# Kernel tuning notes

Measured on AMD Instinct MI355X. Metric: run time of the kernel, lower is better.

## Reference

```python
import jax, jax.numpy as jnp
import numpy as np

# Config (from init_kwargs 'knn')
QUEUE_SIZE = 65536   # K
FEAT_DIM = 256       # D
BATCH = 512          # N (eval_sampling = 1.0 -> all samples used)
NUM_KNNS = 200
NUM_CLASSES = 1000
TEMPERATURE = 0.07


def _l2norm(x):
    return x / jnp.sqrt(jnp.sum(x * x, axis=-1, keepdims=True) + 1e-12)


def setup_inputs() -> dict:
    key = jax.random.key(0)
    k1, k2, k3, k4 = jax.random.split(key, 4)
    features = _l2norm(jax.random.normal(k1, (BATCH, FEAT_DIM), jnp.float32))
    labels = jax.random.randint(k2, (BATCH,), 0, NUM_CLASSES, jnp.int32)
    queue_features = _l2norm(jax.random.normal(k3, (QUEUE_SIZE, FEAT_DIM), jnp.float32))
    queue_labels = jax.random.randint(k4, (QUEUE_SIZE,), 0, NUM_CLASSES, jnp.int32)
    return {
        "features": features,
        "labels": labels,
        "queue_features": queue_features,
        "queue_labels": queue_labels,
        "queue_ptr": 0,
    }


def reference(features, labels, queue_features, queue_labels, queue_ptr):
    # ---- kNN accuracy (train branch, eval_sampling=1.0) ----
    sim = jnp.einsum('nc,kc->nk', features, queue_features)           # [N, K]
    sim_w, sim_idx = jax.lax.top_k(sim, k=NUM_KNNS)                   # [N, Kn]
    sim_w = jnp.exp(sim_w / TEMPERATURE)
    sim_labels = queue_labels[sim_idx]                                # [N, Kn] (vmapped gather)
    # weighted one-hot vote, expressed as a scatter-add (same math,
    # avoids the [N, Kn, C] one-hot intermediate)
    n = features.shape[0]
    pred_scores = jnp.zeros((n, NUM_CLASSES), sim_w.dtype)
    pred_scores = pred_scores.at[jnp.arange(n)[:, None], sim_labels].add(sim_w)
    pred_labels = jnp.argmax(pred_scores, axis=-1)
    accuracy = jnp.mean((pred_labels == labels).astype(jnp.float32))

    # ---- queue update (single device: all_gather == identity) ----
    batch_size = features.shape[0]
    inds = (jnp.arange(batch_size) + queue_ptr) % QUEUE_SIZE  # original asserts divisibility
    new_queue_features = queue_features.at[inds].set(features)
    new_queue_labels = queue_labels.at[inds].set(labels)
    new_queue_ptr = (queue_ptr + batch_size) % QUEUE_SIZE

    return accuracy, new_queue_features, new_queue_labels, new_queue_ptr
```

## Files before the change

### kernel.cpp

```cpp
#include <hip/hip_runtime.h>
#include <math.h>

#define NQ     65536
#define DIM    256
#define NBATCH 512
#define KNN    200
#define NCLS   1000
#define TSELF  0.155f
#define TSELH  0.150f
#define BGUARD 22

#define GM  128
#define GK  32
#define NTN (NQ / GM)
#define KSTEPS (DIM / GK)

typedef unsigned short u16;
typedef unsigned long long u64;
typedef __attribute__((ext_vector_type(8))) short short8;
typedef __attribute__((ext_vector_type(4))) float f32x4;


__device__ __forceinline__ u16 f2bf(float x) {
  unsigned u = __float_as_uint(x);
  return (u16)((u + 0x7FFFu + ((u >> 16) & 1u)) >> 16);
}
__device__ __forceinline__ void load_lds16(const void* g, void* l) {
  __builtin_amdgcn_global_load_lds(
      (const __attribute__((address_space(1))) unsigned int*)g,
      (__attribute__((address_space(3))) unsigned int*)l, 16, 0, 0);
}
__device__ __forceinline__ void store_f4u(float* p, float4 v) {
  p[0] = v.x;
  *(float2*)(p + 1) = make_float2(v.y, v.z);
  p[3] = v.w;
}

__global__ __launch_bounds__(256) void prep_copy_kernel(
    const float* __restrict__ feat, const int* __restrict__ labels,
    const float* __restrict__ qf, const int* __restrict__ ql,
    const int* __restrict__ qptr,
    u16* __restrict__ Bb, u16* __restrict__ Ab,
    int* __restrict__ flag, float* __restrict__ out)
{
  const int idx = blockIdx.x * 256 + threadIdx.x;
  const int ptr = qptr[0];
  const long long NFEAT = (long long)NQ * DIM;

  {
    float4 qv = ((const float4*)qf)[idx];
    int row = idx >> 6;
    int c4  = idx & 63;
    int d = (row - ptr) & (NQ - 1);
    float4 ov = qv;
    if (d < NBATCH) ov = ((const float4*)feat)[d * 64 + c4];
    store_f4u(out + 1 + 4 * (long long)idx, ov);

    ushort4 h;
    h.x = f2bf(qv.x); h.y = f2bf(qv.y); h.z = f2bf(qv.z); h.w = f2bf(qv.w);
    ((ushort4*)Bb)[idx] = h;
  }

  if (idx < NBATCH * DIM / 4) {
    float4 v = ((const float4*)feat)[idx];
    ushort4 h;
    h.x = f2bf(v.x); h.y = f2bf(v.y); h.z = f2bf(v.z); h.w = f2bf(v.w);
    ((ushort4*)Ab)[idx] = h;
  }

  if (idx < NQ) {
    int d = (idx - ptr) & (NQ - 1);
    int v = (d < NBATCH) ? labels[d] : ql[idx];
    out[1 + NFEAT + idx] = (float)v;
  }

  if (idx < NBATCH) flag[idx] = 0;
  if (idx == 0) {
    out[0] = 0.0f;
    out[1 + NFEAT + NQ] = (float)((ptr + NBATCH) & (NQ - 1));
  }
}

__global__ __launch_bounds__(256) void gemm_mfma(
    const u16* __restrict__ A, const u16* __restrict__ B,
    unsigned* __restrict__ cand, int* __restrict__ cnt2,
    int* __restrict__ flag, int SLOT)
{
  __shared__ u16 sA[2][GM][GK];
  __shared__ u16 sB[2][GM][GK];
  __shared__ int lcnt[GM];

  const int tid  = threadIdx.x;
  const int wave = tid >> 6, lane = tid & 63;
  const int d  = blockIdx.x;
  const int bm = (d >> 3) & 3;
  const int bn = (d & 7) | ((d >> 5) << 3);

  for (int i = tid; i < GM; i += 256) lcnt[i] = 0;

  const u16* srcBase = ((wave < 2) ? (A + (size_t)bm * GM * DIM)
                                   : (B + (size_t)bn * GM * DIM))
                       + (size_t)(wave & 1) * 64 * DIM;
  const int kx = ((lane & 3) ^ ((lane >> 3) & 3)) * 8;
  const u16* src = srcBase + (lane >> 2) * DIM + kx;
  u16* dst0 = ((wave < 2) ? &sA[0][0][0] : &sB[0][0][0]) + (wave & 1) * 64 * GK;
  u16* dst1 = ((wave < 2) ? &sA[1][0][0] : &sB[1][0][0]) + (wave & 1) * 64 * GK;

  const int wm = (wave & 1) * 64, wn = (wave >> 1) * 64;
  const int fr = lane & 15;
  const int fq = lane >> 4;
  const int fqx = fq ^ ((fr >> 1) & 3);

  f32x4 acc[4][4] = {};

  {
    const u16* s = src;
#pragma unroll
    for (int g = 0; g < 4; ++g)
      load_lds16(s + g * 16 * DIM, dst0 + g * 512);
  }
  __syncthreads();

  for (int t = 0; t < KSTEPS; ++t) {
    const int cur = t & 1;
    if (t + 1 < KSTEPS) {
      const u16* s = src + (t + 1) * GK;
      u16* dl = cur ? dst0 : dst1;
#pragma unroll
      for (int g = 0; g < 4; ++g)
        load_lds16(s + g * 16 * DIM, dl + g * 512);
    }

    short8 a[4], b[4];
#pragma unroll
    for (int i = 0; i < 4; ++i) {
      a[i] = *(const short8*)&sA[cur][wm + i * 16 + fr][fqx * 8];
      b[i] = *(const short8*)&sB[cur][wn + i * 16 + fr][fqx * 8];
    }
#pragma unroll
    for (int i = 0; i < 4; ++i)
#pragma unroll
      for (int j = 0; j < 4; ++j)
        acc[i][j] = __builtin_amdgcn_mfma_f32_16x16x32_bf16(a[i], b[j], acc[i][j], 0, 0, 0);

    __syncthreads();
  }

  const int lrow0 = wm + fq * 4;
  const int ccol  = bn * GM + wn + fr;
#pragma unroll
  for (int i = 0; i < 4; ++i)
#pragma unroll
    for (int j = 0; j < 4; ++j)
#pragma unroll
      for (int r = 0; r < 4; ++r) {
        float v = acc[i][j][r];
        if (v > TSELF) {
          int lr  = lrow0 + i * 16 + r;
          int col = ccol + j * 16;
          int p = atomicAdd(&lcnt[lr], 1);
          if (p < SLOT)
            cand[((size_t)(bm * GM + lr) * NTN + bn) * SLOT + p] = (unsigned)col;
          else
            flag[bm * GM + lr] = 1;
        }
      }
  __syncthreads();
  if (tid < GM) {
    int c = lcnt[tid];
    cnt2[(size_t)(bm * GM + tid) * NTN + bn] = c < SLOT ? c : SLOT;
  }
}

#define NBSEL 2048
#define CCAP  2048
#define MBCAP 256
#define NT    512
#define NG    (NT / 8)

__global__ __launch_bounds__(NT, 4) void select_kernel(
    const unsigned* __restrict__ cand, const int* __restrict__ cnt2,
    const int* __restrict__ flag, const int* __restrict__ labels,
    const int* __restrict__ qlab, const float* __restrict__ qf,
    const float* __restrict__ feat, float* __restrict__ out,
    float inv_n, int SLOT)
{
  __shared__ int   hist[NBSEL];
  __shared__ int   seg[NT];
  __shared__ float candV[CCAP];
  __shared__ int   candI[CCAP];
  __shared__ float votes[NCLS];
  __shared__ u64   bk[MBCAP];
  __shared__ float frow[DIM];
  __shared__ int   s_b, s_cnt, s_hi, s_mb;
  __shared__ u64   s_best;

  const int tid = threadIdx.x;
  const int row = blockIdx.x;

  bool fb = (flag[row] != 0);

  if (tid < DIM) frow[tid] = feat[(size_t)row * DIM + tid];
  for (int i = tid; i < NBSEL; i += NT) hist[i] = 0;
  for (int c = tid; c < NCLS; c += NT) votes[c] = 0.0f;
  if (tid == 0) { s_b = 0; s_cnt = 0; s_hi = 0; s_mb = 0; s_best = 0ull; }
  __syncthreads();

  if (!fb) {
    const int*      rowcnt  = cnt2 + (size_t)row * NTN;
    const unsigned* rowcand = cand + (size_t)row * NTN * SLOT;
    for (int t = tid; t < NTN; t += NT) {
      int c = rowcnt[t];
      if (c > 0) {
        int p = atomicAdd(&s_cnt, c);
        for (int k = 0; k < c; ++k)
          if (p + k < CCAP) candI[p + k] = (int)rowcand[(size_t)t * SLOT + k];
      }
    }
    __syncthreads();
    const int n = s_cnt;
    if (n < KNN || n > CCAP) fb = true;
    else {
      const int sub = tid & 7;
      const int grp = tid >> 3;
      const float4* fr4 = (const float4*)frow;

      float4 b0[8];
      if (grp < n) {
        const float4* qr = (const float4*)(qf + (size_t)candI[grp] * DIM);
#pragma unroll
        for (int it = 0; it < 8; ++it) b0[it] = qr[sub + it * 8];
      }
      for (int i = grp; i < n; i += NG) {
        const int j = i + NG;
        float4 b1[8];
        if (j < n) {
          const float4* qr = (const float4*)(qf + (size_t)candI[j] * DIM);
#pragma unroll
          for (int it = 0; it < 8; ++it) b1[it] = qr[sub + it * 8];
        }
        float p = 0.0f;
#pragma unroll
        for (int it = 0; it < 8; ++it) {
          float4 a = fr4[sub + it * 8];
          p = fmaf(a.x, b0[it].x, p); p = fmaf(a.y, b0[it].y, p);
          p = fmaf(a.z, b0[it].z, p); p = fmaf(a.w, b0[it].w, p);
        }
        p += __shfl_xor(p, 1, 64);
        p += __shfl_xor(p, 2, 64);
        p += __shfl_xor(p, 4, 64);
        if (sub == 0) candV[i] = p;
#pragma unroll
        for (int it = 0; it < 8; ++it) b0[it] = b1[it];
      }
      __syncthreads();

      const float SSCALE = (float)NBSEL / (1.001f - TSELH);
      for (int i = tid; i < n; i += NT) {
        int b = (int)((candV[i] - TSELH) * SSCALE);
        b = b < 0 ? 0 : (b > NBSEL - 1 ? NBSEL - 1 : b);
        atomicAdd(&hist[b], 1);
      }
      __syncthreads();
      { int s = 0;
#pragma unroll
        for (int i = 0; i < NBSEL / NT; ++i) s += hist[tid * (NBSEL / NT) + i];
        seg[tid] = s; }
      __syncthreads();
      for (int off = 1; off < NT; off <<= 1) {
        int t = (tid + off < NT) ? seg[tid + off] : 0;
        __syncthreads();
        seg[tid] += t;
        __syncthreads();
      }
      { int run = (tid < NT - 1) ? seg[tid + 1] : 0;
        for (int i = tid * (NBSEL / NT) + NBSEL / NT - 1;
             i >= tid * (NBSEL / NT); --i) {
          run += hist[i];
          if (run >= KNN) { atomicMax(&s_b, i); break; }
        } }
      __syncthreads();
      const int bstar = s_b;

      if (bstar < BGUARD) fb = true;
      else {
        for (int i = tid; i < n; i += NT) {
          float v = candV[i];
          int b = (int)((v - TSELH) * SSCALE);
          b = b < 0 ? 0 : (b > NBSEL - 1 ? NBSEL - 1 : b);
          if (b > bstar) {
            atomicAdd(&s_hi, 1);
            atomicAdd(&votes[qlab[candI[i]]], expf(v * (1.0f / 0.07f)));
          } else if (b == bstar) {
            int p = atomicAdd(&s_mb, 1);
            if (p < MBCAP)
              bk[p] = ((u64)__float_as_uint(v) << 32) |
                      (u64)(0xFFFFFFFFu - (unsigned)candI[i]);
          }
        }
        __syncthreads();
        const int mb = s_mb;
        if (mb > MBCAP) fb = true;
        else {
          const int need = KNN - s_hi;
          for (int e = tid; e < mb; e += NT) {
            u64 ke = bk[e];
            int rank = 0;
            for (int j = 0; j < mb; ++j) rank += (bk[j] > ke);
            if (rank < need) {
              float v = __uint_as_float((unsigned)(ke >> 32));
              int col = (int)(0xFFFFFFFFu - (unsigned)(ke & 0xFFFFFFFFull));
              atomicAdd(&votes[qlab[col]], expf(v * (1.0f / 0.07f)));
            }
          }
          __syncthreads();
        }
      }
    }
  }

  if (fb) {
    for (int i = tid; i < NBSEL; i += NT) hist[i] = 0;
    if (tid == 0) { s_b = 0; s_cnt = 0; }
    __syncthreads();

    for (int q = tid; q < NQ; q += NT) {
      const float4* qr = (const float4*)(qf + (size_t)q * DIM);
      const float4* fr = (const float4*)frow;
      float s = 0.0f;
#pragma unroll
      for (int t = 0; t < DIM / 4; ++t) {
        float4 a = fr[t], b = qr[t];
        s = fmaf(a.x, b.x, s); s = fmaf(a.y, b.y, s);
        s = fmaf(a.z, b.z, s); s = fmaf(a.w, b.w, s);
      }
      int bin = (int)((s + 1.0f) * (NBSEL * 0.5f));
      bin = bin < 0 ? 0 : (bin > NBSEL - 1 ? NBSEL - 1 : bin);
      atomicAdd(&hist[bin], 1);
    }
    __syncthreads();

    { int s = 0;
#pragma unroll
      for (int i = 0; i < NBSEL / NT; ++i) s += hist[tid * (NBSEL / NT) + i];
      seg[tid] = s; }
    __syncthreads();
    for (int off = 1; off < NT; off <<= 1) {
      int t = (tid + off < NT) ? seg[tid + off] : 0;
      __syncthreads();
      seg[tid] += t;
      __syncthreads();
    }
    { int run = (tid < NT - 1) ? seg[tid + 1] : 0;
      for (int i = tid * (NBSEL / NT) + NBSEL / NT - 1;
           i >= tid * (NBSEL / NT); --i) {
        run += hist[i];
        if (run >= KNN) { atomicMax(&s_b, i); break; }
      } }
    __syncthreads();
    const int bstar = s_b;

    for (int q = tid; q < NQ; q += NT) {
      const float4* qr = (const float4*)(qf + (size_t)q * DIM);
      const float4* fr = (const float4*)frow;
      float s = 0.0f;
#pragma unroll
      for (int t = 0; t < DIM / 4; ++t) {
        float4 a = fr[t], b = qr[t];
        s = fmaf(a.x, b.x, s); s = fmaf(a.y, b.y, s);
        s = fmaf(a.z, b.z, s); s = fmaf(a.w, b.w, s);
      }
      int bin = (int)((s + 1.0f) * (NBSEL * 0.5f));
      bin = bin < 0 ? 0 : (bin > NBSEL - 1 ? NBSEL - 1 : bin);
      if (bin >= bstar) {
        int p = atomicAdd(&s_cnt, 1);
        if (p < CCAP) { candV[p] = s; candI[p] = q; }
      }
    }
    __syncthreads();
    int m = s_cnt < CCAP ? s_cnt : CCAP;

    int P = 256; while (P < m) P <<= 1;
    for (int i = tid; i < P; i += NT)
      if (i >= m) { candV[i] = -INFINITY; candI[i] = 0x7fffffff; }
    __syncthreads();
    for (int k = 2; k <= P; k <<= 1) {
      for (int j = k >> 1; j > 0; j >>= 1) {
        for (int i = tid; i < P; i += NT) {
          int ixj = i ^ j;
          if (ixj > i) {
            float va = candV[i], vb = candV[ixj];
            int ia = candI[i], ib = candI[ixj];
            bool aFirst = (va > vb) || (va == vb && ia < ib);
            bool up = ((i & k) == 0);
            if (up ? !aFirst : aFirst) {
              candV[i] = vb; candV[ixj] = va;
              candI[i] = ib; candI[ixj] = ia;
            }
          }
        }
        __syncthreads();
      }
    }

    for (int c = tid; c < NCLS; c += NT) votes[c] = 0.0f;
    __syncthreads();
    for (int i = tid; i < KNN; i += NT)
      atomicAdd(&votes[qlab[candI[i]]], expf(candV[i] * (1.0f / 0.07f)));
    __syncthreads();
  }

  u64 key = 0ull;
  for (int c = tid; c < NCLS; c += NT) {
    u64 k2 = ((u64)__float_as_uint(votes[c]) << 32) |
             (u64)(0xFFFFFFFFu - (unsigned)c);
    if (k2 > key) key = k2;
  }
  for (int off = 32; off > 0; off >>= 1) {
    u64 o = __shfl_down(key, off, 64);
    if (o > key) key = o;
  }
  if ((tid & 63) == 0) atomicMax(&s_best, key);
  __syncthreads();
  if (tid == 0) {
    int cls = (int)(0xFFFFFFFFu - (unsigned)(s_best & 0xFFFFFFFFull));
    if (cls == labels[row]) atomicAdd(out, inv_n);
  }
}

extern "C" void kernel_launch(void* const* d_in, const int* in_sizes, int n_in,
                              void* d_out, int out_size, void* d_ws, size_t ws_size,
                              hipStream_t stream)
{
  const float* features = (const float*)d_in[0];
  const int*   labels   = (const int*)d_in[1];
  const float* qfeat    = (const float*)d_in[2];
  const int*   qlab     = (const int*)d_in[3];
  const int*   qptr     = (const int*)d_in[4];
  float* out = (float*)d_out;

  int nbatch = in_sizes[0] / DIM;
  float inv_n = 1.0f / (float)nbatch;

  size_t bBytes = (size_t)NQ * DIM * 2;
  size_t fixed  = bBytes + (size_t)NBATCH * NTN * 4 + NBATCH * 4 +
                  (size_t)NBATCH * DIM * 2;
  int SLOT = 16;
  while ((size_t)NBATCH * NTN * SLOT * 4 + fixed > ws_size && SLOT > 2) SLOT >>= 1;

  u16*      Bb   = (u16*)d_ws;
  unsigned* cand = (unsigned*)((char*)d_ws + bBytes);
  int*      cnt2 = (int*)((char*)cand + (size_t)NBATCH * NTN * SLOT * 4);
  int*      flagp = cnt2 + (size_t)NBATCH * NTN;
  u16*      Ab   = (u16*)(flagp + NBATCH);

  prep_copy_kernel<<<NQ * DIM / 4 / 256, 256, 0, stream>>>(
      features, labels, qfeat, qlab, qptr, Bb, Ab, flagp, out);

  gemm_mfma<<<(NBATCH / GM) * (NQ / GM), 256, 0, stream>>>(
      Ab, Bb, cand, cnt2, flagp, SLOT);

  select_kernel<<<nbatch, NT, 0, stream>>>(cand, cnt2, flagp, labels, qlab,
                                           qfeat, features, out, inv_n, SLOT);
}
```

Baseline: 201.3 us.

## Reuse bf16 GEMM scores to pre-rank candidates, rescore only near-threshold ones in fp32

The GEMM now stores each candidate's bf16 similarity next to its column index. The select kernel builds a histogram from these approximate scores to find a provisional cutoff, keeps only candidates within an error margin of it, and recomputes exact fp32 dot products for that short list before the final exact histogram selection. This cuts the number of gathered 1 KB queue rows and dot products per query, but doubles the candidate buffer size and adds a second histogram and scan pass. Correctness relies on the bf16 error bound EPSF being large enough.

Measured after the change: 200.7 us, median of 2. Within noise of the previous version (-0.3%).

```diff
diff --git a/kernel.cpp b/kernel.cpp
--- a/kernel.cpp
+++ b/kernel.cpp
@@ -8,6 +8,7 @@
 #define NCLS   1000
 #define TSELF  0.155f
 #define TSELH  0.150f
+#define EPSF   0.0041f
 #define BGUARD 22
 
 #define GM  128
@@ -83,7 +84,7 @@
 
 __global__ __launch_bounds__(256) void gemm_mfma(
     const u16* __restrict__ A, const u16* __restrict__ B,
-    unsigned* __restrict__ cand, int* __restrict__ cnt2,
+    uint2* __restrict__ cand, int* __restrict__ cnt2,
     int* __restrict__ flag, int SLOT)
 {
   __shared__ u16 sA[2][GM][GK];
@@ -160,7 +161,8 @@
           int col = ccol + j * 16;
           int p = atomicAdd(&lcnt[lr], 1);
           if (p < SLOT)
-            cand[((size_t)(bm * GM + lr) * NTN + bn) * SLOT + p] = (unsigned)col;
+            cand[((size_t)(bm * GM + lr) * NTN + bn) * SLOT + p] =
+                make_uint2(__float_as_uint(v), (unsigned)col);
           else
             flag[bm * GM + lr] = 1;
         }
@@ -175,11 +177,13 @@
 #define NBSEL 2048
 #define CCAP  2048
 #define MBCAP 256
+#define LCAP  1024
 #define NT    512
 #define NG    (NT / 8)
+#define BINW  ((1.001f - TSELH) / (float)NBSEL)
 
 __global__ __launch_bounds__(NT, 4) void select_kernel(
-    const unsigned* __restrict__ cand, const int* __restrict__ cnt2,
+    const uint2* __restrict__ cand, const int* __restrict__ cnt2,
     const int* __restrict__ flag, const int* __restrict__ labels,
     const int* __restrict__ qlab, const float* __restrict__ qf,
     const float* __restrict__ feat, float* __restrict__ out,
@@ -190,7 +194,7 @@
   __shared__ float candV[CCAP];
   __shared__ int   candI[CCAP];
   __shared__ float votes[NCLS];
-  __shared__ u64   bk[MBCAP];
+  __shared__ u64   bk[LCAP / 2];
   __shared__ float frow[DIM];
   __shared__ int   s_b, s_cnt, s_hi, s_mb;
   __shared__ u64   s_best;
@@ -207,55 +211,26 @@
   __syncthreads();
 
   if (!fb) {
-    const int*      rowcnt  = cnt2 + (size_t)row * NTN;
-    const unsigned* rowcand = cand + (size_t)row * NTN * SLOT;
+    const int*   rowcnt  = cnt2 + (size_t)row * NTN;
+    const uint2* rowcand = cand + (size_t)row * NTN * SLOT;
     for (int t = tid; t < NTN; t += NT) {
       int c = rowcnt[t];
       if (c > 0) {
         int p = atomicAdd(&s_cnt, c);
-        for (int k = 0; k < c; ++k)
-          if (p + k < CCAP) candI[p + k] = (int)rowcand[(size_t)t * SLOT + k];
+        for (int k = 0; k < c; ++k) {
+          if (p + k < CCAP) {
+            uint2 e = rowcand[(size_t)t * SLOT + k];
+            candV[p + k] = __uint_as_float(e.x);
+            candI[p + k] = (int)e.y;
+          }
+        }
       }
     }
     __syncthreads();
     const int n = s_cnt;
     if (n < KNN || n > CCAP) fb = true;
     else {
-      const int sub = tid & 7;
-      const int grp = tid >> 3;
-      const float4* fr4 = (const float4*)frow;
-
-      float4 b0[8];
-      if (grp < n) {
-        const float4* qr = (const float4*)(qf + (size_t)candI[grp] * DIM);
-#pragma unroll
-        for (int it = 0; it < 8; ++it) b0[it] = qr[sub + it * 8];
-      }
-      for (int i = grp; i < n; i += NG) {
-        const int j = i + NG;
-        float4 b1[8];
-        if (j < n) {
-          const float4* qr = (const float4*)(qf + (size_t)candI[j] * DIM);
-#pragma unroll
-          for (int it = 0; it < 8; ++it) b1[it] = qr[sub + it * 8];
-        }
-        float p = 0.0f;
-#pragma unroll
-        for (int it = 0; it < 8; ++it) {
-          float4 a = fr4[sub + it * 8];
-          p = fmaf(a.x, b0[it].x, p); p = fmaf(a.y, b0[it].y, p);
-          p = fmaf(a.z, b0[it].z, p); p = fmaf(a.w, b0[it].w, p);
-        }
-        p += __shfl_xor(p, 1, 64);
-        p += __shfl_xor(p, 2, 64);
-        p += __shfl_xor(p, 4, 64);
-        if (sub == 0) candV[i] = p;
-#pragma unroll
-        for (int it = 0; it < 8; ++it) b0[it] = b1[it];
-      }
-      __syncthreads();
-
-      const float SSCALE = (float)NBSEL / (1.001f - TSELH);
+      const float SSCALE = 1.0f / BINW;
       for (int i = tid; i < n; i += NT) {
         int b = (int)((candV[i] - TSELH) * SSCALE);
         b = b < 0 ? 0 : (b > NBSEL - 1 ? NBSEL - 1 : b);
@@ -280,40 +255,120 @@
           if (run >= KNN) { atomicMax(&s_b, i); break; }
         } }
       __syncthreads();
-      const int bstar = s_b;
-
-      if (bstar < BGUARD) fb = true;
+      const int bstarA = s_b;
+      const float thresh = TSELH + (float)bstarA * BINW - 2.0f * EPSF;
+
+      int* lst = (int*)bk;
+      for (int i = tid; i < NBSEL; i += NT) hist[i] = 0;
+      if (tid == 0) s_b = 0;
+      for (int i = tid; i < n; i += NT) {
+        if (candV[i] >= thresh) {
+          int p = atomicAdd(&s_mb, 1);
+          if (p < LCAP) lst[p] = i;
+        }
+      }
+      __syncthreads();
+      const int nr = s_mb;
+      if (nr > LCAP) fb = true;
       else {
+        const int sub = tid & 7;
+        const int grp = tid >> 3;
+        const float4* fr4 = (const float4*)frow;
+
+        float4 b0[8];
+        if (grp < nr) {
+          const float4* qr = (const float4*)(qf + (size_t)candI[lst[grp]] * DIM);
+#pragma unroll
+          for (int it = 0; it < 8; ++it) b0[it] = qr[sub + it * 8];
+        }
+        for (int k = grp; k < nr; k += NG) {
+          const int kn = k + NG;
+          float4 b1[8];
+          if (kn < nr) {
+            const float4* qr = (const float4*)(qf + (size_t)candI[lst[kn]] * DIM);
+#pragma unroll
+            for (int it = 0; it < 8; ++it) b1[it] = qr[sub + it * 8];
+          }
+          float p = 0.0f;
+#pragma unroll
+          for (int it = 0; it < 8; ++it) {
+            float4 a = fr4[sub + it * 8];
+            p = fmaf(a.x, b0[it].x, p); p = fmaf(a.y, b0[it].y, p);
+            p = fmaf(a.z, b0[it].z, p); p = fmaf(a.w, b0[it].w, p);
+          }
+          p += __shfl_xor(p, 1, 64);
+          p += __shfl_xor(p, 2, 64);
+          p += __shfl_xor(p, 4, 64);
+          if (sub == 0) candV[lst[k]] = p;
+#pragma unroll
+          for (int it = 0; it < 8; ++it) b0[it] = b1[it];
+        }
+        if (tid == 0) s_mb = 0;
+        __syncthreads();
+
         for (int i = tid; i < n; i += NT) {
           float v = candV[i];
-          int b = (int)((v - TSELH) * SSCALE);
-          b = b < 0 ? 0 : (b > NBSEL - 1 ? NBSEL - 1 : b);
-          if (b > bstar) {
-            atomicAdd(&s_hi, 1);
-            atomicAdd(&votes[qlab[candI[i]]], expf(v * (1.0f / 0.07f)));
-          } else if (b == bstar) {
-            int p = atomicAdd(&s_mb, 1);
-            if (p < MBCAP)
-              bk[p] = ((u64)__float_as_uint(v) << 32) |
-                      (u64)(0xFFFFFFFFu - (unsigned)candI[i]);
-          }
-        }
-        __syncthreads();
-        const int mb = s_mb;
-        if (mb > MBCAP) fb = true;
+          if (v >= thresh) {
+            int b = (int)((v - TSELH) * SSCALE);
+            b = b < 0 ? 0 : (b > NBSEL - 1 ? NBSEL - 1 : b);
+            atomicAdd(&hist[b], 1);
+          }
+        }
+        __syncthreads();
+        { int s = 0;
+#pragma unroll
+          for (int i = 0; i < NBSEL / NT; ++i) s += hist[tid * (NBSEL / NT) + i];
+          seg[tid] = s; }
+        __syncthreads();
+        for (int off = 1; off < NT; off <<= 1) {
+          int t = (tid + off < NT) ? seg[tid + off] : 0;
+          __syncthreads();
+          seg[tid] += t;
+          __syncthreads();
+        }
+        { int run = (tid < NT - 1) ? seg[tid + 1] : 0;
+          for (int i = tid * (NBSEL / NT) + NBSEL / NT - 1;
+               i >= tid * (NBSEL / NT); --i) {
+            run += hist[i];
+            if (run >= KNN) { atomicMax(&s_b, i); break; }
+          } }
+        __syncthreads();
+        const int bstar = s_b;
+
+        if (bstar < BGUARD) fb = true;
         else {
-          const int need = KNN - s_hi;
-          for (int e = tid; e < mb; e += NT) {
-            u64 ke = bk[e];
-            int rank = 0;
-            for (int j = 0; j < mb; ++j) rank += (bk[j] > ke);
-            if (rank < need) {
-              float v = __uint_as_float((unsigned)(ke >> 32));
-              int col = (int)(0xFFFFFFFFu - (unsigned)(ke & 0xFFFFFFFFull));
-              atomicAdd(&votes[qlab[col]], expf(v * (1.0f / 0.07f)));
+          for (int i = tid; i < n; i += NT) {
+            float v = candV[i];
+            if (v < thresh) continue;
+            int b = (int)((v - TSELH) * SSCALE);
+            b = b < 0 ? 0 : (b > NBSEL - 1 ? NBSEL - 1 : b);
+            if (b > bstar) {
+              atomicAdd(&s_hi, 1);
+              atomicAdd(&votes[qlab[candI[i]]], expf(v * (1.0f / 0.07f)));
+            } else if (b == bstar) {
+              int p = atomicAdd(&s_mb, 1);
+              if (p < MBCAP)
+                bk[p] = ((u64)__float_as_uint(v) << 32) |
+                        (u64)(0xFFFFFFFFu - (unsigned)candI[i]);
             }
           }
           __syncthreads();
+          const int mb = s_mb;
+          if (mb > MBCAP) fb = true;
+          else {
+            const int need = KNN - s_hi;
+            for (int e = tid; e < mb; e += NT) {
+              u64 ke = bk[e];
+              int rank = 0;
+              for (int j = 0; j < mb; ++j) rank += (bk[j] > ke);
+              if (rank < need) {
+                float v = __uint_as_float((unsigned)(ke >> 32));
+                int col = (int)(0xFFFFFFFFu - (unsigned)(ke & 0xFFFFFFFFull));
+                atomicAdd(&votes[qlab[col]], expf(v * (1.0f / 0.07f)));
+              }
+            }
+            __syncthreads();
+          }
         }
       }
     }
@@ -446,13 +501,13 @@
   size_t fixed  = bBytes + (size_t)NBATCH * NTN * 4 + NBATCH * 4 +
                   (size_t)NBATCH * DIM * 2;
   int SLOT = 16;
-  while ((size_t)NBATCH * NTN * SLOT * 4 + fixed > ws_size && SLOT > 2) SLOT >>= 1;
-
-  u16*      Bb   = (u16*)d_ws;
-  unsigned* cand = (unsigned*)((char*)d_ws + bBytes);
-  int*      cnt2 = (int*)((char*)cand + (size_t)NBATCH * NTN * SLOT * 4);
-  int*      flagp = cnt2 + (size_t)NBATCH * NTN;
-  u16*      Ab   = (u16*)(flagp + NBATCH);
+  while ((size_t)NBATCH * NTN * SLOT * 8 + fixed > ws_size && SLOT > 2) SLOT >>= 1;
+
+  u16*   Bb   = (u16*)d_ws;
+  uint2* cand = (uint2*)((char*)d_ws + bBytes);
+  int*   cnt2 = (int*)((char*)cand + (size_t)NBATCH * NTN * SLOT * 8);
+  int*   flagp = cnt2 + (size_t)NBATCH * NTN;
+  u16*   Ab   = (u16*)(flagp + NBATCH);
 
   prep_copy_kernel<<<NQ * DIM / 4 / 256, 256, 0, stream>>>(
       features, labels, qfeat, qlab, qptr, Bb, Ab, flagp, out);
```
